# Optimization experiments

Measured on AMD Instinct MI355X. Metric: run time of the kernel, lower is better.

## Reference

```python
import jax, jax.numpy as jnp
import numpy as np
import math

NUM_GRAPHS = 256
NODES_PER_GRAPH = 1024
AVG_DEG = 32
D_FEAT = 128
RATIO = 0.8
N_TOTAL = NUM_GRAPHS * NODES_PER_GRAPH
E_TOTAL = N_TOTAL * AVG_DEG


def setup_inputs() -> dict:
    key = jax.random.key(0)
    k1, k2, k3, k4 = jax.random.split(key, 4)
    x = jax.random.normal(k1, (N_TOTAL, D_FEAT), dtype=jnp.float32)
    # intra-graph random edges: local ids in [0, NODES_PER_GRAPH), offset per graph
    e_per = NODES_PER_GRAPH * AVG_DEG
    src_l = jax.random.randint(k2, (NUM_GRAPHS, e_per), 0, NODES_PER_GRAPH)
    dst_l = jax.random.randint(k3, (NUM_GRAPHS, e_per), 0, NODES_PER_GRAPH)
    offs = (jnp.arange(NUM_GRAPHS, dtype=jnp.int64) * NODES_PER_GRAPH)[:, None]
    edge_index = jnp.stack([(src_l + offs).reshape(-1), (dst_l + offs).reshape(-1)], axis=0)
    batch = jnp.repeat(jnp.arange(NUM_GRAPHS, dtype=jnp.int64), NODES_PER_GRAPH)
    W = jax.random.normal(k4, (D_FEAT, 1), dtype=jnp.float32) * (1.0 / math.sqrt(D_FEAT))
    b = jnp.zeros((1,), dtype=jnp.float32)
    return {"x": x, "edge_index": edge_index, "batch": batch, "W": W, "b": b}


def gcn_score(x, edge_index, W, b):
    """GCNConv(in_channels, 1): symmetric-normalized message passing with self-loops."""
    n = x.shape[0]
    xw = x @ W  # [N, 1] -- linear first (out_channels == 1)
    src, dst = edge_index[0], edge_index[1]
    deg = jax.ops.segment_sum(jnp.ones(src.shape[0], dtype=xw.dtype), dst, num_segments=n) + 1.0
    dinv = jax.lax.rsqrt(deg)
    norm = dinv[src] * dinv[dst]  # [E]
    agg = jax.ops.segment_sum(norm[:, None] * xw[src], dst, num_segments=n)
    # self-loop contribution: norm_ii = dinv_i^2 = 1/deg_i
    out = agg + xw * (1.0 / deg)[:, None] + b
    return out.squeeze(-1)  # [N]


def reference(x, edge_index, batch, W, b):
    n = x.shape[0]
    score = gcn_score(x, edge_index, W, b)  # [N]
    # dropout(p=0) is identity -> sc == score
    # per-graph topk (equal-sized graphs, batch is block-contiguous)
    k = math.ceil(RATIO * NODES_PER_GRAPH)
    _, idx = jax.lax.top_k(score.reshape(NUM_GRAPHS, NODES_PER_GRAPH), k)  # desc order, as in PyG topk
    perm = (idx + jnp.arange(NUM_GRAPHS)[:, None] * NODES_PER_GRAPH).reshape(-1)  # [B*k]
    x_ae = x[perm]
    x_out = x_ae * jnp.tanh(score[perm])[:, None]
    new_batch = batch[perm]
    # filter_adj: keep edges with both endpoints retained, reindex to perm positions
    node_map = jnp.full((n,), -1, dtype=edge_index.dtype).at[perm].set(
        jnp.arange(perm.shape[0], dtype=edge_index.dtype))
    src, dst = edge_index[0], edge_index[1]
    edge_mask = (node_map[src] >= 0) & (node_map[dst] >= 0)  # [E] static-shape validity mask
    new_edge_index = jnp.where(edge_mask[None, :], node_map[edge_index], -1)
    return (x_out, new_edge_index, edge_mask, new_batch, perm, x_ae)
```

## Files before the change

### kernel.cpp

```cpp
#include <hip/hip_runtime.h>
#include <math.h>

#define N_TOTAL   262144
#define E_TOTAL   8388608
#define EPG       32768
#define D_FEAT    128
#define NUM_G     256
#define NPG       1024
#define KSEL      820
#define BK        (NUM_G * KSEL)

#define FP_SCALE     4503599627370496.0
#define FP_INV_SCALE (1.0 / FP_SCALE)

typedef float  f32x4 __attribute__((ext_vector_type(4)));
typedef int    i32x4 __attribute__((ext_vector_type(4)));

__global__ void xw_kernel(const float* __restrict__ x, const float* __restrict__ W,
                          double* __restrict__ xw) {
    int gtid = blockIdx.x * blockDim.x + threadIdx.x;
    int node = gtid >> 6;
    int lane = threadIdx.x & 63;
    if (node >= N_TOTAL) return;
    float2 xv = ((const float2*)x)[(size_t)node * 64 + lane];
    float2 wv = ((const float2*)W)[lane];
    double s = (double)xv.x * (double)wv.x + (double)xv.y * (double)wv.y;
    #pragma unroll
    for (int off = 32; off > 0; off >>= 1) s += __shfl_down(s, off, 64);
    if (lane == 0) xw[node] = s;
}

__global__ __launch_bounds__(1024, 1)
void graph_kernel(const int* __restrict__ ei, const double* __restrict__ xw,
                  const float* __restrict__ bptr,
                  int* __restrict__ permInt, float* __restrict__ scaleF,
                  float* __restrict__ out_batch, float* __restrict__ out_perm,
                  float* __restrict__ out_ei0, float* __restrict__ out_ei1,
                  float* __restrict__ out_mask) {
    __shared__ double    mS[NPG];
    __shared__ int       degS[NPG];
    __shared__ double    dinvS[NPG];
    __shared__ long long aggS[NPG];
    __shared__ float     scoreS[NPG];
    __shared__ int       lmap[NPG];

    const int g    = blockIdx.x;
    const int tid  = threadIdx.x;
    const int base = g * NPG;
    const int4* src4 = (const int4*)(ei + (size_t)g * EPG);
    const int4* dst4 = (const int4*)(ei + E_TOTAL + (size_t)g * EPG);

    mS[tid]   = xw[base + tid];
    degS[tid] = 0;
    aggS[tid] = 0;
    __syncthreads();

    #pragma unroll
    for (int k = 0; k < 8; k++) {
        int4 d = dst4[tid + k * 1024];
        atomicAdd(&degS[d.x - base], 1);
        atomicAdd(&degS[d.y - base], 1);
        atomicAdd(&degS[d.z - base], 1);
        atomicAdd(&degS[d.w - base], 1);
    }
    __syncthreads();
    {
        double dinv = 1.0 / sqrt((double)(degS[tid] + 1));
        dinvS[tid] = dinv;
        mS[tid]    = dinv * mS[tid];
    }
    __syncthreads();

    #pragma unroll
    for (int k = 0; k < 8; k++) {
        int4 s = src4[tid + k * 1024];
        int4 d = dst4[tid + k * 1024];
        double tx = mS[s.x - base];
        double ty = mS[s.y - base];
        double tz = mS[s.z - base];
        double tw = mS[s.w - base];
        atomicAdd((unsigned long long*)&aggS[d.x - base], (unsigned long long)(long long)(tx * FP_SCALE));
        atomicAdd((unsigned long long*)&aggS[d.y - base], (unsigned long long)(long long)(ty * FP_SCALE));
        atomicAdd((unsigned long long*)&aggS[d.z - base], (unsigned long long)(long long)(tz * FP_SCALE));
        atomicAdd((unsigned long long*)&aggS[d.w - base], (unsigned long long)(long long)(tw * FP_SCALE));
    }
    __syncthreads();

    {
        double sum = (double)aggS[tid] * FP_INV_SCALE + mS[tid];
        double sc  = dinvS[tid] * sum + (double)bptr[0];
        scoreS[tid] = (float)sc;
    }
    __syncthreads();

    {
        float si = scoreS[tid];
        int rank = 0;
        const float4* s4 = (const float4*)scoreS;
        for (int j = 0; j < NPG / 4; j++) {
            float4 c = s4[j];
            int j0 = j * 4;
            rank += (c.x > si) || (c.x == si && (j0 + 0) < tid);
            rank += (c.y > si) || (c.y == si && (j0 + 1) < tid);
            rank += (c.z > si) || (c.z == si && (j0 + 2) < tid);
            rank += (c.w > si) || (c.w == si && (j0 + 3) < tid);
        }
        int pos = -1;
        if (rank < KSEL) {
            pos = g * KSEL + rank;
            int node = base + tid;
            permInt[pos]   = node;
            scaleF[pos]    = tanhf(si);
            __builtin_nontemporal_store((float)g,    out_batch + pos);
            __builtin_nontemporal_store((float)node, out_perm  + pos);
        }
        lmap[tid] = pos;
    }
    __syncthreads();

    #pragma unroll
    for (int k = 0; k < 8; k++) {
        int idx = tid + k * 1024;
        i32x4 s = __builtin_nontemporal_load((const i32x4*)src4 + idx);
        i32x4 d = __builtin_nontemporal_load((const i32x4*)dst4 + idx);
        f32x4 e0, e1, m;
        int ms, md; bool kp;
        ms = lmap[s.x - base]; md = lmap[d.x - base]; kp = (ms >= 0) && (md >= 0);
        e0.x = kp ? (float)ms : -1.0f; e1.x = kp ? (float)md : -1.0f; m.x = kp ? 1.0f : 0.0f;
        ms = lmap[s.y - base]; md = lmap[d.y - base]; kp = (ms >= 0) && (md >= 0);
        e0.y = kp ? (float)ms : -1.0f; e1.y = kp ? (float)md : -1.0f; m.y = kp ? 1.0f : 0.0f;
        ms = lmap[s.z - base]; md = lmap[d.z - base]; kp = (ms >= 0) && (md >= 0);
        e0.z = kp ? (float)ms : -1.0f; e1.z = kp ? (float)md : -1.0f; m.z = kp ? 1.0f : 0.0f;
        ms = lmap[s.w - base]; md = lmap[d.w - base]; kp = (ms >= 0) && (md >= 0);
        e0.w = kp ? (float)ms : -1.0f; e1.w = kp ? (float)md : -1.0f; m.w = kp ? 1.0f : 0.0f;
        size_t o = (size_t)g * (EPG / 4) + idx;
        __builtin_nontemporal_store(e0, (f32x4*)out_ei0  + o);
        __builtin_nontemporal_store(e1, (f32x4*)out_ei1  + o);
        __builtin_nontemporal_store(m,  (f32x4*)out_mask + o);
    }
}

__global__ void gather_kernel(const float* __restrict__ x, const int* __restrict__ permInt,
                              const float* __restrict__ scaleF,
                              float* __restrict__ out_xout, float* __restrict__ out_xae) {
    int gtid = blockIdx.x * blockDim.x + threadIdx.x;
    int row  = gtid >> 5;
    int lane = gtid & 31;
    if (row >= BK) return;
    int node = permInt[row];
    float t = scaleF[row];
    f32x4 v = *((const f32x4*)x + (size_t)node * 32 + lane);
    f32x4 o = v * t;
    __builtin_nontemporal_store(v, (f32x4*)out_xae  + (size_t)row * 32 + lane);
    __builtin_nontemporal_store(o, (f32x4*)out_xout + (size_t)row * 32 + lane);
}

extern "C" void kernel_launch(void* const* d_in, const int* in_sizes, int n_in,
                              void* d_out, int out_size, void* d_ws, size_t ws_size,
                              hipStream_t stream) {
    const float* x  = (const float*)d_in[0];
    const int*   ei = (const int*)d_in[1];
    const float* W  = (const float*)d_in[3];
    const float* b  = (const float*)d_in[4];

    double* xw      = (double*)d_ws;
    int*    permInt = (int*)(xw + N_TOTAL);
    float*  scaleF  = (float*)(permInt + BK);

    float* out       = (float*)d_out;
    float* out_xout  = out;
    float* out_ei0   = out + (size_t)BK * D_FEAT;
    float* out_ei1   = out_ei0 + E_TOTAL;
    float* out_mask  = out_ei1 + E_TOTAL;
    float* out_batch = out_mask + E_TOTAL;
    float* out_perm  = out_batch + BK;
    float* out_xae   = out_perm + BK;

    xw_kernel<<<(N_TOTAL * 64) / 256, 256, 0, stream>>>(x, W, xw);
    graph_kernel<<<NUM_G, 1024, 0, stream>>>(ei, xw, b, permInt, scaleF,
                                             out_batch, out_perm,
                                             out_ei0, out_ei1, out_mask);
    gather_kernel<<<(BK * 32 + 255) / 256, 256, 0, stream>>>(x, permInt, scaleF,
                                                             out_xout, out_xae);
}
```

Baseline: 514.6 us.

## Fuse score, top-k and gather into one per-graph kernel with radix-bucket ranking

Merges the xw projection, graph scoring, top-k selection and feature gather into a single kernel, one workgroup per graph. This removes two launches and the workspace round trips for xw, perm and scale. The O(N^2) rank loop is replaced by a histogram over key bits plus a prefix scan, so each node only compares against nodes in its own bucket. Destination indices are kept in registers so they are read once instead of three times. In exchange, only 256 workgroups now do all of the x streaming, which may limit memory parallelism. Bucket-based ranking also costs more when scores crowd into a few buckets.

Result: faster. 466.4 us (-9.4%).

```diff
diff --git a/kernel.cpp b/kernel.cpp
--- a/kernel.cpp
+++ b/kernel.cpp
@@ -16,27 +16,14 @@
 typedef float  f32x4 __attribute__((ext_vector_type(4)));
 typedef int    i32x4 __attribute__((ext_vector_type(4)));
 
-__global__ void xw_kernel(const float* __restrict__ x, const float* __restrict__ W,
-                          double* __restrict__ xw) {
-    int gtid = blockIdx.x * blockDim.x + threadIdx.x;
-    int node = gtid >> 6;
-    int lane = threadIdx.x & 63;
-    if (node >= N_TOTAL) return;
-    float2 xv = ((const float2*)x)[(size_t)node * 64 + lane];
-    float2 wv = ((const float2*)W)[lane];
-    double s = (double)xv.x * (double)wv.x + (double)xv.y * (double)wv.y;
-    #pragma unroll
-    for (int off = 32; off > 0; off >>= 1) s += __shfl_down(s, off, 64);
-    if (lane == 0) xw[node] = s;
-}
-
 __global__ __launch_bounds__(1024, 1)
-void graph_kernel(const int* __restrict__ ei, const double* __restrict__ xw,
-                  const float* __restrict__ bptr,
-                  int* __restrict__ permInt, float* __restrict__ scaleF,
-                  float* __restrict__ out_batch, float* __restrict__ out_perm,
-                  float* __restrict__ out_ei0, float* __restrict__ out_ei1,
-                  float* __restrict__ out_mask) {
+void sagpool_fused(const float* __restrict__ x, const int* __restrict__ ei,
+                   const float* __restrict__ Wp, const float* __restrict__ bptr,
+                   float* __restrict__ out_xout, float* __restrict__ out_xae,
+                   float* __restrict__ out_ei0, float* __restrict__ out_ei1,
+                   float* __restrict__ out_mask,
+                   float* __restrict__ out_batch, float* __restrict__ out_perm)
+{
     __shared__ double    mS[NPG];
     __shared__ int       degS[NPG];
     __shared__ double    dinvS[NPG];
@@ -47,21 +34,51 @@
     const int g    = blockIdx.x;
     const int tid  = threadIdx.x;
     const int base = g * NPG;
-    const int4* src4 = (const int4*)(ei + (size_t)g * EPG);
-    const int4* dst4 = (const int4*)(ei + E_TOTAL + (size_t)g * EPG);
-
-    mS[tid]   = xw[base + tid];
+    const i32x4* src4 = (const i32x4*)(ei + (size_t)g * EPG);
+    const i32x4* dst4 = (const i32x4*)(ei + E_TOTAL + (size_t)g * EPG);
+    const float  bb   = bptr[0];
+
     degS[tid] = 0;
     aggS[tid] = 0;
+
+    {
+        const int lane16 = tid & 15;
+        const int rgrp   = tid >> 4;
+        f32x4 w0 = ((const f32x4*)Wp)[lane16 * 2];
+        f32x4 w1 = ((const f32x4*)Wp)[lane16 * 2 + 1];
+        double wd0 = w0.x, wd1 = w0.y, wd2 = w0.z, wd3 = w0.w;
+        double wd4 = w1.x, wd5 = w1.y, wd6 = w1.z, wd7 = w1.w;
+        #pragma unroll
+        for (int p = 0; p < 16; p++) {
+            int row = p * 64 + rgrp;
+            const f32x4* xr = (const f32x4*)(x + (size_t)(base + row) * D_FEAT) + lane16 * 2;
+            f32x4 a = xr[0];
+            f32x4 c = xr[1];
+            double s = (double)a.x * wd0 + (double)a.y * wd1 +
+                       (double)a.z * wd2 + (double)a.w * wd3 +
+                       (double)c.x * wd4 + (double)c.y * wd5 +
+                       (double)c.z * wd6 + (double)c.w * wd7;
+            s += __shfl_xor(s, 8, 16);
+            s += __shfl_xor(s, 4, 16);
+            s += __shfl_xor(s, 2, 16);
+            s += __shfl_xor(s, 1, 16);
+            if (lane16 == 0) mS[row] = s;
+        }
+    }
+
+    i32x4 dreg[8];
+    #pragma unroll
+    for (int k = 0; k < 8; k++)
+        dreg[k] = __builtin_nontemporal_load(dst4 + tid + k * 1024);
+
     __syncthreads();
 
     #pragma unroll
     for (int k = 0; k < 8; k++) {
-        int4 d = dst4[tid + k * 1024];
-        atomicAdd(&degS[d.x - base], 1);
-        atomicAdd(&degS[d.y - base], 1);
-        atomicAdd(&degS[d.z - base], 1);
-        atomicAdd(&degS[d.w - base], 1);
+        atomicAdd(&degS[dreg[k].x - base], 1);
+        atomicAdd(&degS[dreg[k].y - base], 1);
+        atomicAdd(&degS[dreg[k].z - base], 1);
+        atomicAdd(&degS[dreg[k].w - base], 1);
     }
     __syncthreads();
     {
@@ -73,56 +90,111 @@
 
     #pragma unroll
     for (int k = 0; k < 8; k++) {
-        int4 s = src4[tid + k * 1024];
-        int4 d = dst4[tid + k * 1024];
+        i32x4 s = __builtin_nontemporal_load(src4 + tid + k * 1024);
         double tx = mS[s.x - base];
         double ty = mS[s.y - base];
         double tz = mS[s.z - base];
         double tw = mS[s.w - base];
-        atomicAdd((unsigned long long*)&aggS[d.x - base], (unsigned long long)(long long)(tx * FP_SCALE));
-        atomicAdd((unsigned long long*)&aggS[d.y - base], (unsigned long long)(long long)(ty * FP_SCALE));
-        atomicAdd((unsigned long long*)&aggS[d.z - base], (unsigned long long)(long long)(tz * FP_SCALE));
-        atomicAdd((unsigned long long*)&aggS[d.w - base], (unsigned long long)(long long)(tw * FP_SCALE));
-    }
-    __syncthreads();
-
+        atomicAdd((unsigned long long*)&aggS[dreg[k].x - base], (unsigned long long)(long long)(tx * FP_SCALE));
+        atomicAdd((unsigned long long*)&aggS[dreg[k].y - base], (unsigned long long)(long long)(ty * FP_SCALE));
+        atomicAdd((unsigned long long*)&aggS[dreg[k].z - base], (unsigned long long)(long long)(tz * FP_SCALE));
+        atomicAdd((unsigned long long*)&aggS[dreg[k].w - base], (unsigned long long)(long long)(tw * FP_SCALE));
+    }
+    __syncthreads();
+
+    float si;
     {
         double sum = (double)aggS[tid] * FP_INV_SCALE + mS[tid];
-        double sc  = dinvS[tid] * sum + (double)bptr[0];
-        scoreS[tid] = (float)sc;
-    }
-    __syncthreads();
-
-    {
-        float si = scoreS[tid];
-        int rank = 0;
-        const float4* s4 = (const float4*)scoreS;
-        for (int j = 0; j < NPG / 4; j++) {
-            float4 c = s4[j];
-            int j0 = j * 4;
-            rank += (c.x > si) || (c.x == si && (j0 + 0) < tid);
-            rank += (c.y > si) || (c.y == si && (j0 + 1) < tid);
-            rank += (c.z > si) || (c.z == si && (j0 + 2) < tid);
-            rank += (c.w > si) || (c.w == si && (j0 + 3) < tid);
-        }
-        int pos = -1;
-        if (rank < KSEL) {
-            pos = g * KSEL + rank;
-            int node = base + tid;
-            permInt[pos]   = node;
-            scaleF[pos]    = tanhf(si);
-            __builtin_nontemporal_store((float)g,    out_batch + pos);
-            __builtin_nontemporal_store((float)node, out_perm  + pos);
-        }
-        lmap[tid] = pos;
-    }
-    __syncthreads();
+        si = (float)(dinvS[tid] * sum + (double)bb);
+        scoreS[tid] = si;
+    }
+    __syncthreads();
+
+    uint32_t* keyS     = (uint32_t*)aggS;
+    uint32_t* scanB    = keyS + NPG;
+    float*    scaleR   = (float*)scanB;
+    uint32_t* hist     = (uint32_t*)dinvS;
+    uint32_t* scanA    = hist + NPG;
+    int*      mlist    = (int*)mS;
+    int*      cursorS  = mlist + NPG;
+    int*      rankNode = degS;
+
+    uint32_t sb = __float_as_uint(si);
+    if (sb == 0x80000000u) sb = 0u;
+    const uint32_t key = (sb & 0x80000000u) ? ~sb : (sb | 0x80000000u);
+    keyS[tid]    = key;
+    hist[tid]    = 0u;
+    cursorS[tid] = 0;
+    __syncthreads();
+
+    const int bin = (int)(key >> 22);
+    atomicAdd(&hist[bin], 1u);
+    __syncthreads();
+
+    {
+        uint32_t* A = scanA;
+        uint32_t* B = scanB;
+        A[tid] = hist[tid];
+        __syncthreads();
+        #pragma unroll
+        for (int off = 1; off < NPG; off <<= 1) {
+            uint32_t v = A[tid] + ((tid + off < NPG) ? A[tid + off] : 0u);
+            B[tid] = v;
+            __syncthreads();
+            uint32_t* t = A; A = B; B = t;
+        }
+    }
+
+    const int myStart = (int)(scanA[bin] - hist[bin]);
+    {
+        int slot = myStart + atomicAdd(&cursorS[bin], 1);
+        mlist[slot] = tid;
+    }
+    __syncthreads();
+
+    int rank = myStart;
+    {
+        const int h = (int)hist[bin];
+        for (int m = 0; m < h; m++) {
+            int j = mlist[myStart + m];
+            uint32_t kj = keyS[j];
+            rank += (kj > key) || (kj == key && j < tid);
+        }
+    }
+    int pos = -1;
+    if (rank < KSEL) {
+        pos = g * KSEL + rank;
+        rankNode[rank] = tid;
+        scaleR[rank]   = tanhf(si);
+        __builtin_nontemporal_store((float)g,            out_batch + pos);
+        __builtin_nontemporal_store((float)(base + tid), out_perm  + pos);
+    }
+    lmap[tid] = pos;
+    __syncthreads();
+
+    {
+        const int lane32 = tid & 31;
+        const int rowgrp = tid >> 5;
+        #pragma unroll
+        for (int p = 0; p < 26; p++) {
+            int r = p * 32 + rowgrp;
+            if (r < KSEL) {
+                int node = rankNode[r];
+                float t  = scaleR[r];
+                f32x4 v = *((const f32x4*)x + (size_t)(base + node) * 32 + lane32);
+                f32x4 o = v * t;
+                size_t orow = (size_t)(g * KSEL + r) * 32 + lane32;
+                __builtin_nontemporal_store(v, (f32x4*)out_xae  + orow);
+                __builtin_nontemporal_store(o, (f32x4*)out_xout + orow);
+            }
+        }
+    }
 
     #pragma unroll
     for (int k = 0; k < 8; k++) {
         int idx = tid + k * 1024;
-        i32x4 s = __builtin_nontemporal_load((const i32x4*)src4 + idx);
-        i32x4 d = __builtin_nontemporal_load((const i32x4*)dst4 + idx);
+        i32x4 s = __builtin_nontemporal_load(src4 + idx);
+        i32x4 d = dreg[k];
         f32x4 e0, e1, m;
         int ms, md; bool kp;
         ms = lmap[s.x - base]; md = lmap[d.x - base]; kp = (ms >= 0) && (md >= 0);
@@ -140,21 +212,6 @@
     }
 }
 
-__global__ void gather_kernel(const float* __restrict__ x, const int* __restrict__ permInt,
-                              const float* __restrict__ scaleF,
-                              float* __restrict__ out_xout, float* __restrict__ out_xae) {
-    int gtid = blockIdx.x * blockDim.x + threadIdx.x;
-    int row  = gtid >> 5;
-    int lane = gtid & 31;
-    if (row >= BK) return;
-    int node = permInt[row];
-    float t = scaleF[row];
-    f32x4 v = *((const f32x4*)x + (size_t)node * 32 + lane);
-    f32x4 o = v * t;
-    __builtin_nontemporal_store(v, (f32x4*)out_xae  + (size_t)row * 32 + lane);
-    __builtin_nontemporal_store(o, (f32x4*)out_xout + (size_t)row * 32 + lane);
-}
-
 extern "C" void kernel_launch(void* const* d_in, const int* in_sizes, int n_in,
                               void* d_out, int out_size, void* d_ws, size_t ws_size,
                               hipStream_t stream) {
@@ -162,10 +219,6 @@
     const int*   ei = (const int*)d_in[1];
     const float* W  = (const float*)d_in[3];
     const float* b  = (const float*)d_in[4];
-
-    double* xw      = (double*)d_ws;
-    int*    permInt = (int*)(xw + N_TOTAL);
-    float*  scaleF  = (float*)(permInt + BK);
 
     float* out       = (float*)d_out;
     float* out_xout  = out;
@@ -176,10 +229,8 @@
     float* out_perm  = out_batch + BK;
     float* out_xae   = out_perm + BK;
 
-    xw_kernel<<<(N_TOTAL * 64) / 256, 256, 0, stream>>>(x, W, xw);
-    graph_kernel<<<NUM_G, 1024, 0, stream>>>(ei, xw, b, permInt, scaleF,
-                                             out_batch, out_perm,
-                                             out_ei0, out_ei1, out_mask);
-    gather_kernel<<<(BK * 32 + 255) / 256, 256, 0, stream>>>(x, permInt, scaleF,
-                                                             out_xout, out_xae);
+    sagpool_fused<<<NUM_G, 1024, 0, stream>>>(x, ei, W, b,
+                                              out_xout, out_xae,
+                                              out_ei0, out_ei1, out_mask,
+                                              out_batch, out_perm);
 }
```
